# Performance work log

Measured on AMD Instinct MI355X. Metric: run time of the kernel, lower is better.

## Reference

```python
import jax, jax.numpy as jnp
import numpy as np

# ---- static config (matches module defaults / init_kwargs) ----
SX = 256; SY = 256; C = 3; NK = 12; B = 4
R = 10; DT = 0.2; DD = 5; SIGMA = 0.65; THETA_A = 1.0; N_EXP = 2


def _build_kernels():
    """Replicates compute_kernel(): multi-ring Lenia kernels, normalized in real space."""
    rng = np.random.default_rng(42)
    mid = SX // 2
    g = np.mgrid[-mid:mid, -mid:mid]
    dist = np.linalg.norm(g, axis=0)  # [SX, SY]
    Ks = []
    for _ in range(NK):
        r = rng.uniform(0.3, 1.0)
        a = rng.uniform(0.0, 1.0, 3)
        w = rng.uniform(0.05, 0.2, 3)
        b = rng.uniform(0.0, 1.0, 3)
        D = dist / ((R + 15) * r)
        sig = 1.0 / (1.0 + np.exp((D - 1.0) * 10.0))  # sigmoid(-(D-1)*10)
        kerf = (b[None, None, :] * np.exp(-(((D[..., None] - a[None, None, :]) / w[None, None, :]) ** 2) / 2.0)).sum(-1)
        Ks.append(sig * kerf)
    K = np.stack(Ks, axis=-1)  # [SX, SY, NK]
    Kn = K / K.sum(axis=(0, 1), keepdims=True)
    m = rng.uniform(0.05, 0.5, NK)
    s = rng.uniform(0.01, 0.18, NK)
    h = rng.uniform(0.2, 1.0, NK)
    return (Kn.astype(np.float32), m.astype(np.float32), s.astype(np.float32), h.astype(np.float32))


def setup_inputs() -> dict:
    key = jax.random.key(0)
    Kn, m, s, h = _build_kernels()
    A = jax.random.uniform(key, (B, 1, SX, SY, C), dtype=jnp.float32)
    c0 = jnp.asarray(np.arange(NK) % C, dtype=jnp.int32)      # source channel of each kernel
    c1_map = jnp.asarray(np.arange(NK) % C, dtype=jnp.int32)  # target channel of each kernel
    return {"A": A, "Kn": jnp.asarray(Kn), "m": jnp.asarray(m), "s": jnp.asarray(s),
            "h": jnp.asarray(h), "c0": c0, "c1_map": c1_map}


def _sobel(A):
    """Circular (torus) Sobel, separable [1,2,1]x[-1,0,1]/8, on spatial axes (2,3).
    A: [B,1,SX,SY,C] -> [B,1,SX,SY,2,C] (d/dx, d/dy)."""
    sy = jnp.roll(A, -1, 3) + 2.0 * A + jnp.roll(A, 1, 3)
    gx = (jnp.roll(sy, -1, 2) - jnp.roll(sy, 1, 2)) / 8.0
    sx = jnp.roll(A, -1, 2) + 2.0 * A + jnp.roll(A, 1, 2)
    gy = (jnp.roll(sx, -1, 3) - jnp.roll(sx, 1, 3)) / 8.0
    return jnp.stack([gx, gy], axis=4)


def _forward(A, Kn, m, s, h, c0, c1_map):
    # FFT-domain convolution per kernel
    fK = jnp.fft.fft2(jnp.fft.fftshift(Kn, axes=(0, 1)), axes=(0, 1))  # [SX,SY,NK] complex
    fA = jnp.fft.fft2(A, axes=(2, 3))                                   # [B,1,SX,SY,C]
    fAk = fA[..., c0]                                                    # [B,1,SX,SY,NK]
    U = jnp.fft.ifft2(fK[None, None] * fAk, axes=(2, 3)).real           # [B,1,SX,SY,NK]
    # growth(U,m,s) = 2*bell(U,m,s)-1, scaled by h
    G = (2.0 * jnp.exp(-((U - m) ** 2) / (2.0 * s ** 2)) - 1.0) * h
    # sum kernel contributions into their target channel (c1)
    M = jax.nn.one_hot(c1_map, C, dtype=G.dtype)                         # [NK,C]
    Uc = jnp.einsum('bzxyk,kc->bzxyc', G, M)                             # [B,1,SX,SY,C]
    nabla_U = _sobel(Uc)                                                 # [B,1,SX,SY,2,C]
    nabla_A = _sobel(A.sum(-1, keepdims=True))                           # [B,1,SX,SY,2,1]
    alpha = jnp.clip((A[:, :, :, :, None, :] / THETA_A) ** N_EXP, 0.0, 1.0)
    F = nabla_U * (1.0 - alpha) - nabla_A * alpha                        # flow field
    # ---- reintegration tracking (RT) over a (2*DD+1)^2 neighborhood ----
    x = jnp.arange(SX, dtype=F.dtype); y = jnp.arange(SY, dtype=F.dtype)
    pos = jnp.stack(jnp.meshgrid(x, y, indexing='ij'), axis=-1) + 0.5    # [SX,SY,2]
    ma = DD - SIGMA
    mus = pos[None, None, :, :, :, None] + jnp.clip(DT * F, -ma, ma)     # target centers [B,1,SX,SY,2,C]
    offsets = jnp.asarray([(dx, dy) for dx in range(-DD, DD + 1) for dy in range(-DD, DD + 1)], dtype=jnp.int32)
    amax = min(1.0, 2.0 * SIGMA)

    def body(acc, off):
        dx, dy = off[0], off[1]
        rollA = jnp.roll(A, (dx, dy), axis=(2, 3))
        rollmu = jnp.roll(mus, (dx, dy), axis=(2, 3))
        dpmu = jnp.abs(pos[None, None, :, :, :, None] - rollmu)
        sz = 0.5 - dpmu + SIGMA
        area = jnp.prod(jnp.clip(sz, 0.0, amax), axis=4) / (4.0 * SIGMA ** 2)  # [B,1,SX,SY,C]
        return acc + rollA * area, None

    nA, _ = jax.lax.scan(jax.checkpoint(body), jnp.zeros_like(A), offsets)
    return nA


def reference(A, Kn, m, s, h, c0, c1_map):
    return _forward(A, Kn, m, s, h, c0, c1_map)
```

## Files before the change

### kernel.cpp

```cpp
#include <hip/hip_runtime.h>


typedef _Float16 f16;
typedef __attribute__((ext_vector_type(8))) _Float16 half8;
typedef __attribute__((ext_vector_type(16))) float f32x16;

#define RMAX 44
#define NROWS 89
#define NDMAX 8
#define NFRAG (3*NROWS*NDMAX)
#define NBPK ((NFRAG + 4) / 4)
#define ST 168
#define TROWS 120
#define SCHED_STRIDE 1024
#define KTHR 1e-7f

__global__ __launch_bounds__(128) void lenia_meta(const float* __restrict__ Kn,
                                                  int2* __restrict__ meta,
                                                  int* __restrict__ rowr) {
    int blk = blockIdx.x;
    int c = blk / NROWS, ri = blk - c * NROWS;
    int di = ri - RMAX;
    int t = threadIdx.x;
    int dj = t - RMAX;
    int act = 0;
    if (t < NROWS) {
        size_t base = (size_t)(((di + 128) << 8) | (dj + 128)) * 12 + c;
        float k0 = Kn[base], k1 = Kn[base + 3], k2 = Kn[base + 6], k3 = Kn[base + 9];
        act = (fmaxf(fmaxf(k0, k1), fmaxf(k2, k3)) > KTHR) ? 1 : 0;
    }
    __shared__ int smn[128], smx[128];
    smn[t] = act ? dj : 1000;
    smx[t] = act ? dj : -1000;
    __syncthreads();
    for (int s = 64; s > 0; s >>= 1) {
        if (t < s) { smn[t] = min(smn[t], smn[t + s]); smx[t] = max(smx[t], smx[t + s]); }
        __syncthreads();
    }
    if (t == 0) {
        int jmn = smn[0], jmx = smx[0];
        if (jmx < jmn) { meta[blk] = make_int2(1, 0); rowr[blk] = 0; }
        else {
            meta[blk] = make_int2(jmn, jmx);
            rowr[blk] = max(abs(di), max(abs(jmn), abs(jmx)));
        }
    }
}

__global__ __launch_bounds__(128) void lenia_sched(const int2* __restrict__ meta,
                                                   const int* __restrict__ rowr,
                                                   int2* __restrict__ meta2,
                                                   unsigned int* __restrict__ sched,
                                                   int* __restrict__ nsched,
                                                   int* __restrict__ radii) {
    int c = blockIdx.x;
    int t = threadIdx.x;
    __shared__ int pre[NROWS], nds[NROWS], rmx[128];
    int nd = 0, d0 = 0;
    if (t < NROWS) {
        int2 bm = meta[c * NROWS + t];
        if (bm.y >= bm.x) {
            d0 = ((bm.x - 7) >> 3) << 3;
            nd = ((bm.y + 7 - d0) >> 4) + 1;
        }
        meta2[c * NROWS + t] = make_int2(d0, nd);
        nds[t] = nd;
    }
    rmx[t] = (t < NROWS) ? rowr[c * NROWS + t] : 0;
    __syncthreads();
    for (int s = 64; s > 0; s >>= 1) {
        if (t < s) rmx[t] = max(rmx[t], rmx[t + s]);
        __syncthreads();
    }
    __shared__ int tot;
    if (t == 0) {
        radii[c] = rmx[0];
        int acc = 0;
        for (int i = 0; i < NROWS; ++i) { pre[i] = acc; acc += nds[i]; }
        tot = acc;
    }
    __syncthreads();
    if (t < NROWS && nd > 0) {
        int base = pre[t];
        for (int i = 0; i < nd; ++i) {
            int delta = d0 + 16 * i;
            unsigned int off = (unsigned int)(t * ST + delta + 128);
            sched[c * SCHED_STRIDE + base + i] =
                (unsigned int)((c * NROWS + t) * NDMAX + i) | (off << 12);
        }
    }
    if (t == 0) {
        int ns = (tot + 7) & ~7;
        unsigned int padoff = (unsigned int)(RMAX * ST + 128);
        for (int i = tot; i < ns + 48; ++i)
            sched[c * SCHED_STRIDE + i] = (unsigned int)NFRAG | (padoff << 12);
        nsched[c] = ns;
    }
}

__global__ __launch_bounds__(256) void lenia_prep2(const float* __restrict__ Kn,
                                                   const float* __restrict__ A,
                                                   const int2* __restrict__ meta2,
                                                   uint4* __restrict__ bpack,
                                                   f16* __restrict__ Atr) {
    int blk = blockIdx.x;
    if (blk < NBPK) {
        int fi = blk * 4 + (threadIdx.x >> 6);
        int l = threadIdx.x & 63;
        if (fi > NFRAG) return;
        union { f16 h[8]; uint4 u; } pk;
        if (fi == NFRAG) {
            pk.u = make_uint4(0, 0, 0, 0);
            bpack[(size_t)fi * 64 + l] = pk.u;
            return;
        }
        int c = fi / (NROWS * NDMAX);
        int rem = fi - c * (NROWS * NDMAX);
        int ri = rem >> 3, didx = rem & 7;
        int di = ri - RMAX;
        int delta = meta2[c * NROWS + ri].x + 16 * didx;
        int q = (l & 31) >> 3, sy = l & 7, g = l >> 5;
        int dj0 = delta + 8 * g - sy;
        const float* src = Kn + (size_t)(((di + 128) << 8) + (dj0 + 128)) * 12 + c + 3 * q;
        #pragma unroll
        for (int j = 0; j < 8; ++j) pk.h[j] = (f16)src[j * 12];
        bpack[(size_t)fi * 64 + l] = pk.u;
    } else {
        int px = (blk - NBPK) * 256 + threadIdx.x;
        int b = px >> 16, rem = px & 65535;
        const float* ap = A + (size_t)px * 3;
        Atr[(size_t)(b * 3 + 0) * 65536 + rem] = (f16)ap[0];
        Atr[(size_t)(b * 3 + 1) * 65536 + rem] = (f16)ap[1];
        Atr[(size_t)(b * 3 + 2) * 65536 + rem] = (f16)ap[2];
    }
}

__global__ __launch_bounds__(256) void lenia_conv(
        const f16* __restrict__ Atr, const uint4* __restrict__ bpack,
        const unsigned int* __restrict__ sched, const int* __restrict__ nsched,
        const int* __restrict__ radii,
        const float* __restrict__ mp, const float* __restrict__ sp,
        const float* __restrict__ hp, f16* __restrict__ Uc) {
    extern __shared__ f16 smh[];

    const int tid = threadIdx.x;
    const int bc = blockIdx.y;
    const int b = bc / 3, c = bc - b * 3;
    const int x0 = (blockIdx.x >> 3) << 5;
    const int y0 = (blockIdx.x & 7) << 5;

    const int R = __builtin_amdgcn_readfirstlane(min(max(radii[c], 1), RMAX));
    const int R8 = (R + 7) & ~7;
    const int colbase = y0 - R8 - 16;
    const int rows = 32 + 2 * R;
    const f16* Ap = Atr + (size_t)(b * 3 + c) * 65536;

    {
        int nchunk = rows * 21;
        int tr = tid / 21, rem = tid - tr * 21;
        for (int ci = tid; ci < nchunk; ci += 256) {
            int gi = (x0 - R + tr) & 255;
            int gj = (colbase + rem * 8) & 255;
            *(half8*)(smh + tr * ST + rem * 8) = *(const half8*)(Ap + (gi << 8) + gj);
            tr += 12; rem += 4;
            if (rem >= 21) { rem -= 21; ++tr; }
        }
    }
    __syncthreads();

    const int lane = tid & 63, wid = tid >> 6;
    const int m = lane & 31, g = lane >> 5;
    const int abase = (m + R - RMAX) * ST + 8 * wid + R8 + 16 + 8 * g - 128;

    const unsigned int* sW = sched + c * SCHED_STRIDE;
    const int ns = __builtin_amdgcn_readfirstlane(nsched[c]);

    f32x16 accE, accO;
    #pragma unroll
    for (int r = 0; r < 16; ++r) { accE[r] = 0.f; accO[r] = 0.f; }

    int eq[16];
    uint4 bq[16];
    #pragma unroll
    for (int j = 0; j < 16; ++j) {
        int e = __builtin_amdgcn_readfirstlane((int)sW[j]);
        eq[j] = e;
        bq[j] = bpack[(size_t)(e & 4095) * 64 + lane];
    }

    for (int it = 0; it < ns; it += 16) {
        #pragma unroll
        for (int j = 0; j < 16; j += 2) {
            {
                half8 av = *(const half8*)(smh + abase + (eq[j] >> 12));
                union { uint4 u; half8 h; } bb; bb.u = bq[j];
                accE = __builtin_amdgcn_mfma_f32_32x32x16_f16(av, bb.h, accE, 0, 0, 0);
                int ne = __builtin_amdgcn_readfirstlane((int)sW[it + 16 + j]);
                eq[j] = ne;
                bq[j] = bpack[(size_t)(ne & 4095) * 64 + lane];
            }
            {
                half8 av = *(const half8*)(smh + abase + (eq[j + 1] >> 12));
                union { uint4 u; half8 h; } bb; bb.u = bq[j + 1];
                accO = __builtin_amdgcn_mfma_f32_32x32x16_f16(av, bb.h, accO, 0, 0, 0);
                int ne = __builtin_amdgcn_readfirstlane((int)sW[it + 17 + j]);
                eq[j + 1] = ne;
                bq[j + 1] = bpack[(size_t)(ne & 4095) * 64 + lane];
            }
        }
    }

    const int q = (lane & 31) >> 3, sy = lane & 7;
    const float mq = mp[c + 3 * q];
    const float sq = sp[c + 3 * q];
    const float hq = hp[c + 3 * q];
    const float i2s = 1.f / (2.f * sq * sq);
    #pragma unroll
    for (int r = 0; r < 16; ++r) {
        float d = (accE[r] + accO[r]) - mq;
        float gg = (2.f * expf(-d * d * i2s) - 1.f) * hq;
        gg += __shfl_xor(gg, 8);
        gg += __shfl_xor(gg, 16);
        if ((lane & 24) == 0) {
            int row = (r & 3) + ((r >> 2) << 3) + (g << 2);
            Uc[((size_t)(b << 16) + ((x0 + row) << 8) + (y0 + 8 * wid + sy)) * 3 + c] = (f16)gg;
        }
    }
}

#define FTW 44
#define FSW 45
#define PLH (FSW * FTW)
__global__ __launch_bounds__(256) void lenia_flowrt(
        const f16* __restrict__ Atr, const f16* __restrict__ Uc,
        float* __restrict__ out) {
    extern __shared__ char fraw[];
    f16*    ucp = (f16*)fraw;
    f16*    atp = (f16*)(fraw + PLH * 2);
    float2* muq = (float2*)(fraw + 8 * PLH);

    int bc = blockIdx.y;
    int b = bc / 3, c = bc - b * 3;
    int t = blockIdx.x;
    int x0 = (t >> 3) << 5, y0 = (t & 7) << 5;
    const f16* A0 = Atr + (size_t)(b * 3) * 65536;
    const f16* Ub = Uc + ((size_t)b << 16) * 3;

    for (int idx = threadIdx.x; idx < FTW * FTW; idx += 256) {
        int si = idx / FTW, sj = idx - si * FTW;
        int gi = (x0 - 6 + si) & 255, gj = (y0 - 6 + sj) & 255;
        int pix = (gi << 8) + gj;
        int o = si * FSW + sj;
        ucp[o] = Ub[(size_t)pix * 3 + c];
        atp[o] = A0[pix];
        atp[PLH + o] = A0[65536 + pix];
        atp[2 * PLH + o] = A0[131072 + pix];
    }
    __syncthreads();

    for (int idx = threadIdx.x; idx < 42 * 42; idx += 256) {
        int ci = idx / 42, cj = idx - ci * 42;
        int si = ci + 1, sj = cj + 1;
        int o = si * FSW + sj;
        int vx = x0 - 6 + si, vy = y0 - 6 + sj;
        float sx = (vx < 0 || vx > 255) ? 1e7f : 0.f;
        float syv = (vy < 0 || vy > 255) ? 1e7f : 0.f;

        float as[3][3];
        #pragma unroll
        for (int i = 0; i < 3; ++i)
            #pragma unroll
            for (int j = 0; j < 3; ++j) {
                int oo = o + (i - 1) * FSW + (j - 1);
                as[i][j] = (float)atp[oo] + (float)atp[PLH + oo] + (float)atp[2 * PLH + oo];
            }
        float gxA = ((as[2][0] + 2.f * as[2][1] + as[2][2])
                   - (as[0][0] + 2.f * as[0][1] + as[0][2])) * 0.125f;
        float gyA = ((as[0][2] + 2.f * as[1][2] + as[2][2])
                   - (as[0][0] + 2.f * as[1][0] + as[2][0])) * 0.125f;

        float u00 = ucp[o - FSW - 1], u01 = ucp[o - FSW], u02 = ucp[o - FSW + 1];
        float u10 = ucp[o - 1],                          u12 = ucp[o + 1];
        float u20 = ucp[o + FSW - 1], u21 = ucp[o + FSW], u22 = ucp[o + FSW + 1];
        float gx = ((u20 + 2.f * u21 + u22) - (u00 + 2.f * u01 + u02)) * 0.125f;
        float gy = ((u02 + 2.f * u12 + u22) - (u00 + 2.f * u10 + u20)) * 0.125f;
        float a = (float)atp[c * PLH + o];
        float alpha = fminf(a * a, 1.f);
        float Fx = gx * (1.f - alpha) - gxA * alpha;
        float Fy = gy * (1.f - alpha) - gyA * alpha;
        float dx = fminf(fmaxf(0.2f * Fx, -4.35f), 4.35f) + sx;
        float dy = fminf(fmaxf(0.2f * Fy, -4.35f), 4.35f) + syv;
        muq[o] = make_float2(dx, dy);
    }
    __syncthreads();

    int tx = threadIdx.x & 31, tyg = threadIdx.x >> 5;
    int ty0 = tyg << 2;
    float a0 = 0.f, a1 = 0.f, a2 = 0.f, a3 = 0.f;
    const f16* ac = atp + c * PLH;

    for (int dxs = 0; dxs < 11; ++dxs) {
        float fdx = (float)(5 - dxs);
        int rowb = (tx + 1 + dxs) * FSW + (ty0 + 1);
        #pragma unroll
        for (int sjj = 0; sjj < 14; ++sjj) {
            float fdy = (float)(5 - sjj);
            float2 mu = muq[rowb + sjj];
            float av = (float)ac[rowb + sjj];
            float wx = fminf(fmaxf(1.15f - fabsf(fdx - mu.x), 0.f), 1.f);
            float awx = av * wx;
            float e0 = fdy - mu.y;
            a0 = fmaf(awx, fminf(fmaxf(1.15f - fabsf(e0), 0.f), 1.f), a0);
            a1 = fmaf(awx, fminf(fmaxf(1.15f - fabsf(e0 + 1.f), 0.f), 1.f), a1);
            a2 = fmaf(awx, fminf(fmaxf(1.15f - fabsf(e0 + 2.f), 0.f), 1.f), a2);
            a3 = fmaf(awx, fminf(fmaxf(1.15f - fabsf(e0 + 3.f), 0.f), 1.f), a3);
        }
    }
    const float inv = 1.0f / 1.69f;
    size_t ob = ((size_t)(b << 16) + ((x0 + tx) << 8) + (y0 + ty0)) * 3 + c;
    out[ob]     = a0 * inv;
    out[ob + 3] = a1 * inv;
    out[ob + 6] = a2 * inv;
    out[ob + 9] = a3 * inv;
}

extern "C" void kernel_launch(void* const* d_in, const int* in_sizes, int n_in,
                              void* d_out, int out_size, void* d_ws, size_t ws_size,
                              hipStream_t stream) {
    const float* A  = (const float*)d_in[0];
    const float* Kn = (const float*)d_in[1];
    const float* m  = (const float*)d_in[2];
    const float* s  = (const float*)d_in[3];
    const float* h  = (const float*)d_in[4];

    char* ws = (char*)d_ws;
    int*          radii = (int*)ws;
    int*          nschd = (int*)(ws + 16);
    int*          rowr  = (int*)(ws + 64);
    int2*         meta  = (int2*)(ws + 2048);
    int2*         meta2 = (int2*)(ws + 8192);
    unsigned int* sched = (unsigned int*)(ws + 16384);
    f16*          Atr   = (f16*)(ws + 32768);
    uint4*        bpack = (uint4*)(ws + 1605632);
    f16*          Uc    = (f16*)(ws + 3793920);

    lenia_meta<<<3 * NROWS, 128, 0, stream>>>(Kn, meta, rowr);
    lenia_sched<<<3, 128, 0, stream>>>(meta, rowr, meta2, sched, nschd, radii);
    lenia_prep2<<<NBPK + 1024, 256, 0, stream>>>(Kn, A, meta2, bpack, Atr);
    lenia_conv<<<dim3(64, 12), 256, TROWS * ST * sizeof(f16), stream>>>(
        Atr, bpack, sched, nschd, radii, m, s, h, Uc);
    lenia_flowrt<<<dim3(64, 12), 256, 8 * PLH + PLH * 8, stream>>>(
        Atr, Uc, (float*)d_out);
}
```

Measured before the change: 74.67 us.

## Split convolution schedule across wave pairs and reuse B fragments for two column tiles

Each wave now computes two adjacent 8-column output tiles with one B fragment load, so every global bpack fetch feeds two MFMAs instead of one. The schedule is split in half between paired waves, which adds a shared-memory reduction of accumulators and an extra barrier before the Gaussian growth epilogue. Schedule padding is rounded to 16 so the halves align with the 8-deep prefetch. The goal is to halve B-operand global traffic per MFMA, at the cost of the LDS reduction and the epilogue running on only half the waves.

```diff
diff --git a/kernel.cpp b/kernel.cpp
--- a/kernel.cpp
+++ b/kernel.cpp
@@ -90,7 +90,7 @@
         }
     }
     if (t == 0) {
-        int ns = (tot + 7) & ~7;
+        int ns = (tot + 15) & ~15;
         unsigned int padoff = (unsigned int)(RMAX * ST + 128);
         for (int i = tot; i < ns + 48; ++i)
             sched[c * SCHED_STRIDE + i] = (unsigned int)NFRAG | (padoff << 12);
@@ -169,61 +169,75 @@
     __syncthreads();
 
     const int lane = tid & 63, wid = tid >> 6;
+    const int h = wid & 1, p = wid >> 1;
     const int m = lane & 31, g = lane >> 5;
-    const int abase = (m + R - RMAX) * ST + 8 * wid + R8 + 16 + 8 * g - 128;
-
-    const unsigned int* sW = sched + c * SCHED_STRIDE;
+    const int abase = (m + R - RMAX) * ST + 16 * p + R8 + 16 + 8 * g - 128;
+
     const int ns = __builtin_amdgcn_readfirstlane(nsched[c]);
-
-    f32x16 accE, accO;
+    const int nsH = ns >> 1;
+    const unsigned int* sW = sched + c * SCHED_STRIDE + h * nsH;
+
+    f32x16 accA, accB;
     #pragma unroll
-    for (int r = 0; r < 16; ++r) { accE[r] = 0.f; accO[r] = 0.f; }
-
-    int eq[16];
-    uint4 bq[16];
+    for (int r = 0; r < 16; ++r) { accA[r] = 0.f; accB[r] = 0.f; }
+
+    int eq[8];
+    uint4 bq[8];
     #pragma unroll
-    for (int j = 0; j < 16; ++j) {
+    for (int j = 0; j < 8; ++j) {
         int e = __builtin_amdgcn_readfirstlane((int)sW[j]);
         eq[j] = e;
         bq[j] = bpack[(size_t)(e & 4095) * 64 + lane];
     }
 
-    for (int it = 0; it < ns; it += 16) {
-        #pragma unroll
-        for (int j = 0; j < 16; j += 2) {
-            {
-                half8 av = *(const half8*)(smh + abase + (eq[j] >> 12));
-                union { uint4 u; half8 h; } bb; bb.u = bq[j];
-                accE = __builtin_amdgcn_mfma_f32_32x32x16_f16(av, bb.h, accE, 0, 0, 0);
-                int ne = __builtin_amdgcn_readfirstlane((int)sW[it + 16 + j]);
-                eq[j] = ne;
-                bq[j] = bpack[(size_t)(ne & 4095) * 64 + lane];
+    for (int it = 0; it < nsH; it += 8) {
+        #pragma unroll
+        for (int j = 0; j < 8; ++j) {
+            const int off = abase + (eq[j] >> 12);
+            half8 a0 = *(const half8*)(smh + off);
+            half8 a1 = *(const half8*)(smh + off + 8);
+            union { uint4 u; half8 h; } bb; bb.u = bq[j];
+            accA = __builtin_amdgcn_mfma_f32_32x32x16_f16(a0, bb.h, accA, 0, 0, 0);
+            accB = __builtin_amdgcn_mfma_f32_32x32x16_f16(a1, bb.h, accB, 0, 0, 0);
+            int ne = __builtin_amdgcn_readfirstlane((int)sW[it + 8 + j]);
+            eq[j] = ne;
+            bq[j] = bpack[(size_t)(ne & 4095) * 64 + lane];
+        }
+    }
+
+    __syncthreads();
+    float* red = (float*)smh;
+    if (h == 1) {
+        float* dst = red + ((size_t)(p * 64 + lane)) * 33;
+        #pragma unroll
+        for (int r = 0; r < 16; ++r) { dst[r] = accA[r]; dst[16 + r] = accB[r]; }
+    }
+    __syncthreads();
+    if (h == 0) {
+        const float* src = red + ((size_t)(p * 64 + lane)) * 33;
+        #pragma unroll
+        for (int r = 0; r < 16; ++r) { accA[r] += src[r]; accB[r] += src[16 + r]; }
+
+        const int q = (lane & 31) >> 3, sy = lane & 7;
+        const float mq = mp[c + 3 * q];
+        const float sq = sp[c + 3 * q];
+        const float hq = hp[c + 3 * q];
+        const float i2s = 1.f / (2.f * sq * sq);
+        #pragma unroll
+        for (int oo = 0; oo < 2; ++oo) {
+            const f32x16& acc = oo ? accB : accA;
+            const int col = y0 + 16 * p + 8 * oo + sy;
+            #pragma unroll
+            for (int r = 0; r < 16; ++r) {
+                float d = acc[r] - mq;
+                float gg = (2.f * expf(-d * d * i2s) - 1.f) * hq;
+                gg += __shfl_xor(gg, 8);
+                gg += __shfl_xor(gg, 16);
+                if ((lane & 24) == 0) {
+                    int row = (r & 3) + ((r >> 2) << 3) + (g << 2);
+                    Uc[((size_t)(b << 16) + ((x0 + row) << 8) + col) * 3 + c] = (f16)gg;
+                }
             }
-            {
-                half8 av = *(const half8*)(smh + abase + (eq[j + 1] >> 12));
-                union { uint4 u; half8 h; } bb; bb.u = bq[j + 1];
-                accO = __builtin_amdgcn_mfma_f32_32x32x16_f16(av, bb.h, accO, 0, 0, 0);
-                int ne = __builtin_amdgcn_readfirstlane((int)sW[it + 17 + j]);
-                eq[j + 1] = ne;
-                bq[j + 1] = bpack[(size_t)(ne & 4095) * 64 + lane];
-            }
-        }
-    }
-
-    const int q = (lane & 31) >> 3, sy = lane & 7;
-    const float mq = mp[c + 3 * q];
-    const float sq = sp[c + 3 * q];
-    const float hq = hp[c + 3 * q];
-    const float i2s = 1.f / (2.f * sq * sq);
-    #pragma unroll
-    for (int r = 0; r < 16; ++r) {
-        float d = (accE[r] + accO[r]) - mq;
-        float gg = (2.f * expf(-d * d * i2s) - 1.f) * hq;
-        gg += __shfl_xor(gg, 8);
-        gg += __shfl_xor(gg, 16);
-        if ((lane & 24) == 0) {
-            int row = (r & 3) + ((r >> 2) << 3) + (g << 2);
-            Uc[((size_t)(b << 16) + ((x0 + row) << 8) + (y0 + 8 * wid + sy)) * 3 + c] = (f16)gg;
         }
     }
 }
```

Result: no change. 74.40 us (-0.4%).
